# Kernel optimization log

Hardware: AMD Instinct MI355X
Metric: run time of the kernel (lower is better)

The kernel has to match this reference:

```python
import jax, jax.numpy as jnp
import numpy as np

NUM_EMBEDDINGS = 1024
EMBEDDING_DIM = 64


def setup_inputs() -> dict:
    key = jax.random.key(0)
    k1, k2 = jax.random.split(key)
    z = jax.random.normal(k1, (64, 32, 32, EMBEDDING_DIM), dtype=jnp.float32)
    # torch init: uniform_(-1/num_embeddings, 1/num_embeddings)
    lim = 1.0 / NUM_EMBEDDINGS
    codebook = jax.random.uniform(
        k2, (NUM_EMBEDDINGS, EMBEDDING_DIM), dtype=jnp.float32,
        minval=-lim, maxval=lim)
    return {"z": z, "codebook": codebook}


def reference(z, codebook):
    # z: [..., D]; codebook: [K, D]
    z_flat = z.reshape(-1, z.shape[-1])                      # [N, D]
    # ||z||^2 - 2 z.e + ||e||^2  -> [N, K]
    distances = (
        jnp.sum(z_flat ** 2, axis=1, keepdims=True)
        - 2.0 * jnp.einsum("nd,kd->nk", z_flat, codebook)
        + jnp.sum(codebook ** 2, axis=1)
    )
    min_indices = jnp.argmin(distances, axis=1)              # [N]
    z_q = jnp.take(codebook, min_indices, axis=0).reshape(z.shape)
    return z_q, min_indices
```

## Files before the change

kernel.cpp:

```cpp
#include <hip/hip_runtime.h>
#include <hip/hip_bf16.h>
#include <math.h>


#define D      64
#define K      1024

typedef _Float16 half8_t __attribute__((ext_vector_type(8)));
typedef float    floatx4 __attribute__((ext_vector_type(4)));
typedef unsigned long long u64;

#define WS_CN_OFF 0
#define WS_EF_OFF 4096

__device__ __forceinline__ float np_sumsq64_p(const float* __restrict__ x) {
    float r[8];
    {
        float4 v0 = *(const float4*)(x);
        float4 v1 = *(const float4*)(x + 4);
        r[0] = __fmul_rn(v0.x, v0.x); r[1] = __fmul_rn(v0.y, v0.y);
        r[2] = __fmul_rn(v0.z, v0.z); r[3] = __fmul_rn(v0.w, v0.w);
        r[4] = __fmul_rn(v1.x, v1.x); r[5] = __fmul_rn(v1.y, v1.y);
        r[6] = __fmul_rn(v1.z, v1.z); r[7] = __fmul_rn(v1.w, v1.w);
    }
#pragma unroll
    for (int i = 8; i < 64; i += 8) {
        float4 v0 = *(const float4*)(x + i);
        float4 v1 = *(const float4*)(x + i + 4);
        r[0] = __fadd_rn(r[0], __fmul_rn(v0.x, v0.x));
        r[1] = __fadd_rn(r[1], __fmul_rn(v0.y, v0.y));
        r[2] = __fadd_rn(r[2], __fmul_rn(v0.z, v0.z));
        r[3] = __fadd_rn(r[3], __fmul_rn(v0.w, v0.w));
        r[4] = __fadd_rn(r[4], __fmul_rn(v1.x, v1.x));
        r[5] = __fadd_rn(r[5], __fmul_rn(v1.y, v1.y));
        r[6] = __fadd_rn(r[6], __fmul_rn(v1.z, v1.z));
        r[7] = __fadd_rn(r[7], __fmul_rn(v1.w, v1.w));
    }
    return __fadd_rn(__fadd_rn(__fadd_rn(r[0], r[1]), __fadd_rn(r[2], r[3])),
                     __fadd_rn(__fadd_rn(r[4], r[5]), __fadd_rn(r[6], r[7])));
}

__global__ void vq_pre(const float* __restrict__ cb, float* __restrict__ cn,
                       _Float16* __restrict__ ef) {
    const int k = blockIdx.x * 64 + threadIdx.x;
    if (k >= K) return;
    cn[k] = np_sumsq64_p(cb + (long)k * D);
    const int t = k >> 6, ct = (k >> 4) & 3, l16 = k & 15;
#pragma unroll
    for (int ch = 0; ch < 2; ++ch)
#pragma unroll
        for (int quad = 0; quad < 4; ++quad) {
            const float* p = cb + (long)k * D + ch * 32 + quad * 8;
            half8_t h1, h2;
#pragma unroll
            for (int j = 0; j < 8; ++j) {
                float x10 = __fmul_rn(p[j], 1024.0f);
                _Float16 g1 = (_Float16)x10;
                h1[j] = g1;
                h2[j] = (_Float16)(__fmul_rn(__fsub_rn(x10, (float)g1), 2048.0f));
            }
            const int base = t * 8192 + 128 * quad + 8 * l16;
            *(half8_t*)(ef + base + 512 * (ch * 4 + ct))       = h1;
            *(half8_t*)(ef + base + 512 * ((2 + ch) * 4 + ct)) = h2;
        }
}

__global__ __launch_bounds__(1024) void vq_main(
    const float* __restrict__ z, const float* __restrict__ cb,
    const _Float16* __restrict__ ef, const float* __restrict__ cn,
    float* __restrict__ zq, float* __restrict__ idx_out) {
    __shared__ __align__(16) float    zf[128 * 68];
    __shared__ __align__(16) _Float16 za[8 * 2048];
    __shared__ float sS[128];
    __shared__ u64   smerge[128 * 18];
    __shared__ int   sBi[128];

    const int tid  = threadIdx.x;
    const int lane = tid & 63;
    const int wv   = tid >> 6;
    const int quad = lane >> 4;
    const int l16  = lane & 15;
    const long rowbase = (long)blockIdx.x * 128;

    const _Float16* myef = ef + wv * 8192;
    half8_t b1[4][2], b2[4][2];
#pragma unroll
    for (int ct = 0; ct < 4; ++ct)
#pragma unroll
        for (int ch = 0; ch < 2; ++ch) {
            b1[ct][ch] = *(const half8_t*)(myef + 512 * (ch * 4 + ct) + 8 * lane);
            b2[ct][ch] = *(const half8_t*)(myef + 512 * ((2 + ch) * 4 + ct) + 8 * lane);
        }
    const int kl = wv * 64 + l16;
    float mycn[4];
#pragma unroll
    for (int ct = 0; ct < 4; ++ct) mycn[ct] = cn[kl + ct * 16];

    const float4* gz = (const float4*)(z + rowbase * D);
#pragma unroll
    for (int i = 0; i < 2; ++i) {
        int idx4 = i * 1024 + tid;
        int r = idx4 >> 4, j = idx4 & 15;
        *(float4*)(zf + r * 68 + j * 4) = gz[idx4];
    }
    __syncthreads();

    if (lane < 8) sS[wv * 8 + lane] = np_sumsq64_p(zf + (wv * 8 + lane) * 68);

    {
        const int t = wv >> 1, spl = wv & 1;
#pragma unroll
        for (int ch = 0; ch < 2; ++ch) {
            const float* p = zf + (t * 16 + l16) * 68 + ch * 32 + quad * 8;
            float4 f0 = *(const float4*)(p);
            float4 f1 = *(const float4*)(p + 4);
            float xs[8] = {f0.x, f0.y, f0.z, f0.w, f1.x, f1.y, f1.z, f1.w};
            half8_t h;
#pragma unroll
            for (int j = 0; j < 8; ++j) {
                _Float16 h1 = (_Float16)xs[j];
                h[j] = spl ? (_Float16)(__fmul_rn(__fsub_rn(xs[j], (float)h1), 2048.0f))
                           : h1;
            }
            *(half8_t*)(za + t * 2048 + (spl * 2 + ch) * 512 + 8 * lane) = h;
        }
    }
    __syncthreads();

    const double INF_KEY = __builtin_bit_cast(double, 0x7F800000FFFFFFFFull);

    for (int t = 0; t < 8; ++t) {
        half8_t a1[2], a2[2];
#pragma unroll
        for (int ch = 0; ch < 2; ++ch) {
            a1[ch] = *(const half8_t*)(za + t * 2048 + ch * 512 + 8 * lane);
            a2[ch] = *(const half8_t*)(za + t * 2048 + (2 + ch) * 512 + 8 * lane);
        }
        float4 Sv4 = *(const float4*)(sS + t * 16 + quad * 4);
        float Sarr[4] = {Sv4.x, Sv4.y, Sv4.z, Sv4.w};
        double best[4] = {INF_KEY, INF_KEY, INF_KEY, INF_KEY};

#pragma unroll
        for (int ct = 0; ct < 4; ++ct) {
            floatx4 aM = (floatx4){0.f, 0.f, 0.f, 0.f};
            floatx4 aC = (floatx4){0.f, 0.f, 0.f, 0.f};
#pragma unroll
            for (int ch = 0; ch < 2; ++ch) {
                aM = __builtin_amdgcn_mfma_f32_16x16x32_f16(a1[ch], b1[ct][ch], aM, 0, 0, 0);
                aC = __builtin_amdgcn_mfma_f32_16x16x32_f16(a1[ch], b2[ct][ch], aC, 0, 0, 0);
                aC = __builtin_amdgcn_mfma_f32_16x16x32_f16(a2[ch], b1[ct][ch], aC, 0, 0, 0);
            }
            const unsigned kg = (unsigned)(kl + ct * 16);
#pragma unroll
            for (int r = 0; r < 4; ++r) {
                float ds = fmaf(aC[r], 0x1p-11f, aM[r]);
                float t2 = __fmul_rn(ds, 0x1p-9f);
                float dist = __fadd_rn(__fsub_rn(Sarr[r], t2), mycn[ct]);
                uint2 u; u.x = kg; u.y = __float_as_uint(dist);
                best[r] = fmin(best[r], __builtin_bit_cast(double, u));
            }
        }
#pragma unroll
        for (int r = 0; r < 4; ++r) {
            double v = best[r];
#pragma unroll
            for (int off = 1; off <= 8; off <<= 1)
                v = fmin(v, __shfl_xor(v, off));
            if (l16 == 0)
                smerge[(t * 16 + quad * 4 + r) * 18 + wv] = __builtin_bit_cast(u64, v);
        }
    }
    __syncthreads();

    if (lane < 8) {
        const int row = wv * 8 + lane;
        const u64* m = smerge + row * 18;
        double v = __builtin_bit_cast(double, m[0]);
#pragma unroll
        for (int i = 1; i < 16; ++i)
            v = fmin(v, __builtin_bit_cast(double, m[i]));
        const unsigned kbest = (unsigned)(__builtin_bit_cast(u64, v) & 0xFFFFFFFFull);
        sBi[row] = (int)kbest;
        idx_out[rowbase + row] = (float)kbest;
    }
    __syncthreads();

    {
        const int row = tid >> 3, j = tid & 7;
        const int kk = sBi[row];
        const float4* src = (const float4*)(cb + (long)kk * D);
        float4* dst = (float4*)(zq + (rowbase + row) * D);
        dst[j * 2]     = src[j * 2];
        dst[j * 2 + 1] = src[j * 2 + 1];
    }
}

extern "C" void kernel_launch(void* const* d_in, const int* in_sizes, int n_in,
                              void* d_out, int out_size, void* d_ws, size_t ws_size,
                              hipStream_t stream) {
    const float* z  = (const float*)d_in[0];
    const float* cb = (const float*)d_in[1];

    const int n_rows = in_sizes[0] / D;
    float* zq      = (float*)d_out;
    float* idx_out = zq + (long)n_rows * D;

    float*    ws_cn = (float*)((char*)d_ws + WS_CN_OFF);
    _Float16* ws_ef = (_Float16*)((char*)d_ws + WS_EF_OFF);

    vq_pre<<<K / 64, 64, 0, stream>>>(cb, ws_cn, ws_ef);
    vq_main<<<n_rows / 128, 1024, 0, stream>>>(z, cb, ws_ef, ws_cn, zq, idx_out);
}
```

Baseline: 115.6 us.

## Shrink blocks to 32 rows and 4 waves, looping over codebook chunks

Each block now covers 32 rows with 256 threads instead of 128 rows with 1024 threads. Every wave loops over four codebook chunks, loading that chunk's split-fp16 B fragments each iteration, and keeps running argmin keys for two row tiles in registers. Smaller blocks give four times as many workgroups for load balancing and less LDS per block. In exchange the codebook fragments are reloaded from global or L2 memory per chunk rather than held in registers for the whole block. The final gather is rewritten as a coalesced float4 loop.

```diff
diff --git a/kernel.cpp b/kernel.cpp
--- a/kernel.cpp
+++ b/kernel.cpp
@@ -5,6 +5,7 @@
 
 #define D      64
 #define K      1024
+#define BLOCK  256
 
 typedef _Float16 half8_t __attribute__((ext_vector_type(8)));
 typedef float    floatx4 __attribute__((ext_vector_type(4)));
@@ -65,47 +66,33 @@
         }
 }
 
-__global__ __launch_bounds__(1024) void vq_main(
+__global__ __launch_bounds__(BLOCK, 2) void vq_main(
     const float* __restrict__ z, const float* __restrict__ cb,
     const _Float16* __restrict__ ef, const float* __restrict__ cn,
     float* __restrict__ zq, float* __restrict__ idx_out) {
-    __shared__ __align__(16) float    zf[128 * 68];
-    __shared__ __align__(16) _Float16 za[8 * 2048];
-    __shared__ float sS[128];
-    __shared__ u64   smerge[128 * 18];
-    __shared__ int   sBi[128];
+    __shared__ __align__(16) float    zf[32 * 68];
+    __shared__ __align__(16) _Float16 za[2 * 2048];
+    __shared__ float sS[32];
+    __shared__ u64   smerge[32 * 4];
+    __shared__ int   sBi[32];
 
     const int tid  = threadIdx.x;
     const int lane = tid & 63;
     const int wv   = tid >> 6;
     const int quad = lane >> 4;
     const int l16  = lane & 15;
-    const long rowbase = (long)blockIdx.x * 128;
-
-    const _Float16* myef = ef + wv * 8192;
-    half8_t b1[4][2], b2[4][2];
-#pragma unroll
-    for (int ct = 0; ct < 4; ++ct)
-#pragma unroll
-        for (int ch = 0; ch < 2; ++ch) {
-            b1[ct][ch] = *(const half8_t*)(myef + 512 * (ch * 4 + ct) + 8 * lane);
-            b2[ct][ch] = *(const half8_t*)(myef + 512 * ((2 + ch) * 4 + ct) + 8 * lane);
-        }
-    const int kl = wv * 64 + l16;
-    float mycn[4];
-#pragma unroll
-    for (int ct = 0; ct < 4; ++ct) mycn[ct] = cn[kl + ct * 16];
+    const long rowbase = (long)blockIdx.x * 32;
 
     const float4* gz = (const float4*)(z + rowbase * D);
 #pragma unroll
     for (int i = 0; i < 2; ++i) {
-        int idx4 = i * 1024 + tid;
+        int idx4 = i * BLOCK + tid;
         int r = idx4 >> 4, j = idx4 & 15;
         *(float4*)(zf + r * 68 + j * 4) = gz[idx4];
     }
     __syncthreads();
 
-    if (lane < 8) sS[wv * 8 + lane] = np_sumsq64_p(zf + (wv * 8 + lane) * 68);
+    if (tid < 32) sS[tid] = np_sumsq64_p(zf + tid * 68);
 
     {
         const int t = wv >> 1, spl = wv & 1;
@@ -127,71 +114,98 @@
     }
     __syncthreads();
 
+    float Sv[2][4];
+#pragma unroll
+    for (int t = 0; t < 2; ++t) {
+        float4 s4 = *(const float4*)(sS + t * 16 + quad * 4);
+        Sv[t][0] = s4.x; Sv[t][1] = s4.y; Sv[t][2] = s4.z; Sv[t][3] = s4.w;
+    }
+
     const double INF_KEY = __builtin_bit_cast(double, 0x7F800000FFFFFFFFull);
-
-    for (int t = 0; t < 8; ++t) {
-        half8_t a1[2], a2[2];
-#pragma unroll
-        for (int ch = 0; ch < 2; ++ch) {
-            a1[ch] = *(const half8_t*)(za + t * 2048 + ch * 512 + 8 * lane);
-            a2[ch] = *(const half8_t*)(za + t * 2048 + (2 + ch) * 512 + 8 * lane);
-        }
-        float4 Sv4 = *(const float4*)(sS + t * 16 + quad * 4);
-        float Sarr[4] = {Sv4.x, Sv4.y, Sv4.z, Sv4.w};
-        double best[4] = {INF_KEY, INF_KEY, INF_KEY, INF_KEY};
-
-#pragma unroll
-        for (int ct = 0; ct < 4; ++ct) {
-            floatx4 aM = (floatx4){0.f, 0.f, 0.f, 0.f};
-            floatx4 aC = (floatx4){0.f, 0.f, 0.f, 0.f};
+    double best[2][4];
+#pragma unroll
+    for (int t = 0; t < 2; ++t)
+#pragma unroll
+        for (int r = 0; r < 4; ++r) best[t][r] = INF_KEY;
+
+    for (int c = 0; c < 4; ++c) {
+        const _Float16* tb = ef + (c * 4 + wv) * 8192 + 8 * lane;
+        half8_t b1[4][2], b2[4][2];
+#pragma unroll
+        for (int ct = 0; ct < 4; ++ct)
 #pragma unroll
             for (int ch = 0; ch < 2; ++ch) {
-                aM = __builtin_amdgcn_mfma_f32_16x16x32_f16(a1[ch], b1[ct][ch], aM, 0, 0, 0);
-                aC = __builtin_amdgcn_mfma_f32_16x16x32_f16(a1[ch], b2[ct][ch], aC, 0, 0, 0);
-                aC = __builtin_amdgcn_mfma_f32_16x16x32_f16(a2[ch], b1[ct][ch], aC, 0, 0, 0);
-            }
-            const unsigned kg = (unsigned)(kl + ct * 16);
-#pragma unroll
-            for (int r = 0; r < 4; ++r) {
-                float ds = fmaf(aC[r], 0x1p-11f, aM[r]);
-                float t2 = __fmul_rn(ds, 0x1p-9f);
-                float dist = __fadd_rn(__fsub_rn(Sarr[r], t2), mycn[ct]);
-                uint2 u; u.x = kg; u.y = __float_as_uint(dist);
-                best[r] = fmin(best[r], __builtin_bit_cast(double, u));
-            }
-        }
+                b1[ct][ch] = *(const half8_t*)(tb + 512 * (ch * 4 + ct));
+                b2[ct][ch] = *(const half8_t*)(tb + 512 * ((2 + ch) * 4 + ct));
+            }
+        const int kb = c * 256 + wv * 64 + l16;
+        float mycn[4];
+#pragma unroll
+        for (int ct = 0; ct < 4; ++ct) mycn[ct] = cn[kb + ct * 16];
+
+#pragma unroll
+        for (int t = 0; t < 2; ++t) {
+            half8_t a1[2], a2[2];
+#pragma unroll
+            for (int ch = 0; ch < 2; ++ch) {
+                a1[ch] = *(const half8_t*)(za + t * 2048 + ch * 512 + 8 * lane);
+                a2[ch] = *(const half8_t*)(za + t * 2048 + (2 + ch) * 512 + 8 * lane);
+            }
+#pragma unroll
+            for (int ct = 0; ct < 4; ++ct) {
+                floatx4 aM = (floatx4){0.f, 0.f, 0.f, 0.f};
+                floatx4 aC = (floatx4){0.f, 0.f, 0.f, 0.f};
+#pragma unroll
+                for (int ch = 0; ch < 2; ++ch) {
+                    aM = __builtin_amdgcn_mfma_f32_16x16x32_f16(a1[ch], b1[ct][ch], aM, 0, 0, 0);
+                    aC = __builtin_amdgcn_mfma_f32_16x16x32_f16(a1[ch], b2[ct][ch], aC, 0, 0, 0);
+                    aC = __builtin_amdgcn_mfma_f32_16x16x32_f16(a2[ch], b1[ct][ch], aC, 0, 0, 0);
+                }
+                const unsigned kg = (unsigned)(kb + ct * 16);
+#pragma unroll
+                for (int r = 0; r < 4; ++r) {
+                    float ds = fmaf(aC[r], 0x1p-11f, aM[r]);
+                    float t2 = __fmul_rn(ds, 0x1p-9f);
+                    float dist = __fadd_rn(__fsub_rn(Sv[t][r], t2), mycn[ct]);
+                    uint2 u; u.x = kg; u.y = __float_as_uint(dist);
+                    best[t][r] = fmin(best[t][r], __builtin_bit_cast(double, u));
+                }
+            }
+        }
+    }
+
+#pragma unroll
+    for (int t = 0; t < 2; ++t)
 #pragma unroll
         for (int r = 0; r < 4; ++r) {
-            double v = best[r];
+            double v = best[t][r];
 #pragma unroll
             for (int off = 1; off <= 8; off <<= 1)
                 v = fmin(v, __shfl_xor(v, off));
             if (l16 == 0)
-                smerge[(t * 16 + quad * 4 + r) * 18 + wv] = __builtin_bit_cast(u64, v);
-        }
-    }
-    __syncthreads();
-
-    if (lane < 8) {
-        const int row = wv * 8 + lane;
-        const u64* m = smerge + row * 18;
+                smerge[(t * 16 + quad * 4 + r) * 4 + wv] = __builtin_bit_cast(u64, v);
+        }
+    __syncthreads();
+
+    if (tid < 32) {
+        const u64* m = smerge + tid * 4;
         double v = __builtin_bit_cast(double, m[0]);
 #pragma unroll
-        for (int i = 1; i < 16; ++i)
+        for (int i = 1; i < 4; ++i)
             v = fmin(v, __builtin_bit_cast(double, m[i]));
         const unsigned kbest = (unsigned)(__builtin_bit_cast(u64, v) & 0xFFFFFFFFull);
-        sBi[row] = (int)kbest;
-        idx_out[rowbase + row] = (float)kbest;
-    }
-    __syncthreads();
-
-    {
-        const int row = tid >> 3, j = tid & 7;
-        const int kk = sBi[row];
-        const float4* src = (const float4*)(cb + (long)kk * D);
-        float4* dst = (float4*)(zq + (rowbase + row) * D);
-        dst[j * 2]     = src[j * 2];
-        dst[j * 2 + 1] = src[j * 2 + 1];
+        sBi[tid] = (int)kbest;
+        idx_out[rowbase + tid] = (float)kbest;
+    }
+    __syncthreads();
+
+    const float4* cb4 = (const float4*)cb;
+    float4* zq4 = (float4*)(zq + rowbase * D);
+#pragma unroll
+    for (int i = 0; i < 2; ++i) {
+        int idx4 = i * BLOCK + tid;
+        int r = idx4 >> 4, j = idx4 & 15;
+        zq4[idx4] = cb4[(long)sBi[r] * 16 + j];
     }
 }
 
@@ -209,5 +223,5 @@
     _Float16* ws_ef = (_Float16*)((char*)d_ws + WS_EF_OFF);
 
     vq_pre<<<K / 64, 64, 0, stream>>>(cb, ws_cn, ws_ef);
-    vq_main<<<n_rows / 128, 1024, 0, stream>>>(z, cb, ws_ef, ws_cn, zq, idx_out);
-}
+    vq_main<<<n_rows / 32, BLOCK, 0, stream>>>(z, cb, ws_ef, ws_cn, zq, idx_out);
+}
```

Measured after the change: 107.8 us. 1.07x faster.
